# Performance work log

Hardware: AMD Instinct MI355X
Metric: run time of the kernel (lower is better)

## Reference

```python
import jax, jax.numpy as jnp
import numpy as np

D_MODEL = 512
NUM_HEADS = 8
D_K = D_MODEL // NUM_HEADS


def setup_inputs() -> dict:
    key = jax.random.key(0)
    ks = jax.random.split(key, 9)
    B, T = 4, 2048
    s = 1.0 / np.sqrt(D_MODEL)
    inp = {"x": jax.random.normal(ks[0], (B, T, D_MODEL), dtype=jnp.float32)}
    names = ["wq", "wk", "wv", "wo"]
    for i, n in enumerate(names):
        inp[n] = jax.random.uniform(ks[1 + i], (D_MODEL, D_MODEL), dtype=jnp.float32, minval=-s, maxval=s)
        inp["b" + n[1]] = jax.random.uniform(ks[5 + i], (D_MODEL,), dtype=jnp.float32, minval=-s, maxval=s)
    return inp


def reference(x, wq, bq, wk, bk, wv, bv, wo, bo):
    B, T, C = x.shape
    # Linear projections (torch Linear: x @ W^T + b)
    q = x @ wq.T + bq
    k = x @ wk.T + bk
    v = x @ wv.T + bv
    # [B, H, T, d_k]
    q = q.reshape(B, T, NUM_HEADS, D_K).transpose(0, 2, 1, 3)
    k = k.reshape(B, T, NUM_HEADS, D_K).transpose(0, 2, 1, 3)
    v = v.reshape(B, T, NUM_HEADS, D_K).transpose(0, 2, 1, 3)
    # scaled dot-product attention, full [B,H,T,T] scores materialized (faithful)
    scores = jnp.einsum('bhqd,bhkd->bhqk', q, k) / jnp.sqrt(jnp.float32(D_K))
    weights = jax.nn.softmax(scores, axis=-1)
    attn = jnp.einsum('bhqk,bhkd->bhqd', weights, v)
    attn = attn.transpose(0, 2, 1, 3).reshape(B, T, C)
    return attn @ wo.T + bo
```

## Files before the change

### kernel.cpp

```cpp
#include <hip/hip_runtime.h>

typedef __bf16 bf16x8 __attribute__((ext_vector_type(8)));
typedef __bf16 bf16x4 __attribute__((ext_vector_type(4)));
typedef float f32x4 __attribute__((ext_vector_type(4)));
typedef float f32x16 __attribute__((ext_vector_type(16)));

#define MFMA_16x16x32(a, b, c) __builtin_amdgcn_mfma_f32_16x16x32_bf16((a), (b), (c), 0, 0, 0)
#define MFMA32(a, b, c) __builtin_amdgcn_mfma_f32_32x32x16_bf16((a), (b), (c), 0, 0, 0)

#define WAIT_LGKM0() do { \
    asm volatile("s_waitcnt lgkmcnt(0)" ::: "memory"); \
    __builtin_amdgcn_sched_barrier(0); } while (0)

typedef const __attribute__((address_space(1))) void GVp;
typedef __attribute__((address_space(3))) void LVp;
#define GLOAD16(gp, lp) \
    __builtin_amdgcn_global_load_lds((GVp*)(gp), (LVp*)(lp), 16, 0, 0)

__device__ __forceinline__ float fexp2(float x) {
    float r;
    asm("v_exp_f32 %0, %1" : "=v"(r) : "v"(x));
    return r;
}

__device__ __forceinline__ unsigned cvtpk(float lo, float hi) {
    unsigned r;
    asm("v_cvt_pk_bf16_f32 %0, %1, %2" : "=v"(r) : "v"(lo), "v"(hi));
    return r;
}
#define PSWAP(a, b) asm volatile("v_permlane32_swap_b32 %0, %1" : "+v"(a), "+v"(b))

union PB { unsigned u[4]; bf16x8 v; };

__device__ __forceinline__ int swz(int row, int colb) {
    return row * 128 + (colb ^ ((row & 7) << 4));
}

__global__ __launch_bounds__(256) void cvt_all(const float* __restrict__ x,
                                               const float* __restrict__ w0,
                                               const float* __restrict__ w1,
                                               const float* __restrict__ w2,
                                               const float* __restrict__ w3,
                                               __bf16* __restrict__ xo,
                                               __bf16* __restrict__ o0,
                                               __bf16* __restrict__ o1,
                                               __bf16* __restrict__ o2,
                                               __bf16* __restrict__ o3) {
    int i = blockIdx.x * 256 + threadIdx.x;
    const float* in;
    __bf16* out;
    int idx;
    if (i < 1048576) {
        in = x; out = xo; idx = i;
    } else {
        int j = i - 1048576;
        int s = j >> 16;
        idx = j & 65535;
        in = (s == 0) ? w0 : (s == 1) ? w1 : (s == 2) ? w2 : w3;
        out = (s == 0) ? o0 : (s == 1) ? o1 : (s == 2) ? o2 : o3;
    }
    float4 v = ((const float4*)in)[idx];
    bf16x4 o;
    o[0] = (__bf16)v.x; o[1] = (__bf16)v.y; o[2] = (__bf16)v.z; o[3] = (__bf16)v.w;
    ((bf16x4*)out)[idx] = o;
}

template <typename OT, bool VT, int BN>
__device__ __forceinline__ void gemm_body(const __bf16* __restrict__ A,
                                          const __bf16* __restrict__ Bw,
                                          const float* __restrict__ bias,
                                          OT* __restrict__ C,
                                          int K, int N, float scale) {
    const int m0 = blockIdx.x * 128;
    const int n0 = blockIdx.y * BN;
    const int tid = threadIdx.x;
    const int l = tid & 63, w = tid >> 6;
    constexpr int MI = (BN == 128) ? 4 : 2;
    constexpr int WMS = (BN == 128) ? 64 : 32;
    const int wr = (BN == 128) ? (w >> 1) : w;
    const int wc = (BN == 128) ? (w & 1) : 0;
    const int lr = l & 15;
    const int lkb = (l >> 4) << 4;

    __shared__ __bf16 As[128 * 64];
    __shared__ __bf16 Bs[BN * 64];
    char* AsC = (char*)As;
    char* BsC = (char*)Bs;

    const int srow = tid >> 3;
    const int c8 = ((tid & 7) ^ (srow & 7)) * 8;

    f32x4 acc[MI][4] = {};

    for (int k0 = 0; k0 < K; k0 += 64) {
        __syncthreads();
#pragma unroll
        for (int p = 0; p < 4; ++p) {
            int row = p * 32 + srow;
            GLOAD16(A + (size_t)(m0 + row) * K + k0 + c8, AsC + p * 4096 + tid * 16);
        }
#pragma unroll
        for (int p = 0; p < BN / 32; ++p) {
            int row = p * 32 + srow;
            GLOAD16(Bw + (size_t)(n0 + row) * K + k0 + c8, BsC + p * 4096 + tid * 16);
        }
        __syncthreads();
#pragma unroll
        for (int kk = 0; kk < 2; ++kk) {
            bf16x8 af[MI], bfr[4];
#pragma unroll
            for (int mi = 0; mi < MI; ++mi)
                af[mi] = *(const bf16x8*)(AsC + swz(wr * WMS + mi * 16 + lr, kk * 64 + lkb));
#pragma unroll
            for (int ni = 0; ni < 4; ++ni)
                bfr[ni] = *(const bf16x8*)(BsC + swz(wc * 64 + ni * 16 + lr, kk * 64 + lkb));
#pragma unroll
            for (int mi = 0; mi < MI; ++mi)
#pragma unroll
                for (int ni = 0; ni < 4; ++ni)
                    acc[mi][ni] = MFMA_16x16x32(af[mi], bfr[ni], acc[mi][ni]);
        }
    }

    const int rb = (l >> 4) * 4;
#pragma unroll
    for (int mi = 0; mi < MI; ++mi) {
#pragma unroll
        for (int ni = 0; ni < 4; ++ni) {
            int gn = n0 + wc * 64 + ni * 16 + lr;
            int gm = m0 + wr * WMS + mi * 16 + rb;
            float bv = bias[gn];
            if constexpr (VT) {
                bf16x4 o4;
#pragma unroll
                for (int j = 0; j < 4; ++j)
                    o4[j] = (__bf16)((acc[mi][ni][j] + bv) * scale);
                *(bf16x4*)((__bf16*)C + ((size_t)(gm >> 11) << 20) +
                           (size_t)gn * 2048 + (gm & 2047)) = o4;
            } else {
#pragma unroll
                for (int j = 0; j < 4; ++j) {
                    float v = (acc[mi][ni][j] + bv) * scale;
                    C[(size_t)(gm + j) * N + gn] = (OT)v;
                }
            }
        }
    }
}

#define QSCALE 0.18033688f

__global__ __launch_bounds__(256) void qkv_gemm(const __bf16* __restrict__ X,
                                                const __bf16* __restrict__ Wq,
                                                const __bf16* __restrict__ Wk,
                                                const __bf16* __restrict__ Wv,
                                                const float* __restrict__ bq,
                                                const float* __restrict__ bk,
                                                const float* __restrict__ bv,
                                                __bf16* __restrict__ Qo,
                                                __bf16* __restrict__ Ko,
                                                __bf16* __restrict__ Vto) {
    int z = blockIdx.z;
    if (z == 0) {
        gemm_body<__bf16, false, 128>(X, Wq, bq, Qo, 512, 512, QSCALE);
    } else if (z == 1) {
        gemm_body<__bf16, false, 128>(X, Wk, bk, Ko, 512, 512, 1.0f);
    } else {
        gemm_body<__bf16, true, 128>(X, Wv, bv, Vto, 512, 512, 1.0f);
    }
}

__global__ __launch_bounds__(256) void out_gemm_fused(const __bf16* __restrict__ Op0,
                                                      const __bf16* __restrict__ Op1,
                                                      const float* __restrict__ lsum,
                                                      const __bf16* __restrict__ W,
                                                      const float* __restrict__ bias,
                                                      float* __restrict__ C) {
    const int m0 = blockIdx.x * 64;
    const int n0 = blockIdx.y * 128;
    const int tid = threadIdx.x;
    const int l = tid & 63, w = tid >> 6;
    const int wr = w >> 1, wc = w & 1;
    const int lr = l & 15;
    const int lkb = (l >> 4) << 4;

    __shared__ __bf16 As[64 * 64];
    __shared__ __bf16 Bs[128 * 64];
    __shared__ float2 wts[8][64];
    char* AsC = (char*)As;
    char* BsC = (char*)Bs;

    const int b = m0 >> 11, q0 = m0 & 2047;

#pragma unroll
    for (int j = 0; j < 2; ++j) {
        int idx = tid + j * 256;
        int i = idx & 63, hh = idx >> 6;
        size_t r = (size_t)(b * 8 + hh) * 2048 + q0 + i;
        float l0v = lsum[r], l1v = lsum[65536 + r];
        float inv = 1.f / (l0v + l1v);
        wts[hh][i] = make_float2(l0v * inv, l1v * inv);
    }

    const int srow = tid >> 3;
    const int c8 = ((tid & 7) ^ (srow & 7)) * 8;

    f32x4 acc[2][4] = {};

    for (int k0 = 0; k0 < 512; k0 += 64) {
        __syncthreads();
        const int hh = k0 >> 6;
#pragma unroll
        for (int p = 0; p < 2; ++p) {
            int row = p * 32 + srow;
            size_t r = (size_t)(b * 8 + hh) * 2048 + q0 + row;
            float2 wt = wts[hh][row];
            bf16x8 o0 = *(const bf16x8*)(Op0 + r * 64 + c8);
            bf16x8 o1 = *(const bf16x8*)(Op1 + r * 64 + c8);
            bf16x8 mg;
#pragma unroll
            for (int jj = 0; jj < 8; ++jj)
                mg[jj] = (__bf16)((float)o0[jj] * wt.x + (float)o1[jj] * wt.y);
            *(bf16x8*)(AsC + p * 4096 + tid * 16) = mg;
        }
#pragma unroll
        for (int p = 0; p < 4; ++p)
            GLOAD16(W + (size_t)(n0 + p * 32 + srow) * 512 + k0 + c8,
                    BsC + p * 4096 + tid * 16);
        __syncthreads();
#pragma unroll
        for (int kk = 0; kk < 2; ++kk) {
            bf16x8 af[2], bfr[4];
#pragma unroll
            for (int mi = 0; mi < 2; ++mi)
                af[mi] = *(const bf16x8*)(AsC + swz(wr * 32 + mi * 16 + lr, kk * 64 + lkb));
#pragma unroll
            for (int ni = 0; ni < 4; ++ni)
                bfr[ni] = *(const bf16x8*)(BsC + swz(wc * 64 + ni * 16 + lr, kk * 64 + lkb));
#pragma unroll
            for (int mi = 0; mi < 2; ++mi)
#pragma unroll
                for (int ni = 0; ni < 4; ++ni)
                    acc[mi][ni] = MFMA_16x16x32(af[mi], bfr[ni], acc[mi][ni]);
        }
    }

    const int rb = (l >> 4) * 4;
#pragma unroll
    for (int mi = 0; mi < 2; ++mi) {
#pragma unroll
        for (int ni = 0; ni < 4; ++ni) {
            int gn = n0 + wc * 64 + ni * 16 + lr;
            int gm = m0 + wr * 32 + mi * 16 + rb;
            float bv = bias[gn];
#pragma unroll
            for (int j = 0; j < 4; ++j)
                C[(size_t)(gm + j) * 512 + gn] = acc[mi][ni][j] + bv;
        }
    }
}

__global__ __launch_bounds__(256, 2) void attn_fwd(const __bf16* __restrict__ Q,
                                                   const __bf16* __restrict__ K,
                                                   const __bf16* __restrict__ Vt,
                                                   __bf16* __restrict__ Op0,
                                                   __bf16* __restrict__ Op1,
                                                   float* __restrict__ lsum) {
    const int T = 2048, Cm = 512;
    const int qt0 = blockIdx.x * 128;
    const int h = blockIdx.y;
    const int half = blockIdx.z & 1, b = blockIdx.z >> 1;
    const int kt0 = half * 1024, kend = kt0 + 1024;
    const int tid = threadIdx.x;
    const int l = tid & 63, w = tid >> 6;
    const int q5 = l & 31, hi = l >> 5;
    const size_t rbase = ((size_t)b * T) * Cm + h * 64;
    const size_t vtbase = ((size_t)b << 20) + (size_t)(h * 64) * 2048;

    __shared__ __align__(16) char smem[33280];

    const int grow = tid >> 3;
    const int gcol = ((tid & 7) ^ (grow & 7)) * 8;
    const __bf16* kgp = K + rbase + (size_t)grow * Cm + gcol;
    const __bf16* vgp = Vt + vtbase + (size_t)grow * 2048 + gcol;

#define ATTN_STAGE(nb, ktv)                                                   \
    do {                                                                      \
        char* kd_ = smem + (nb) * 8192 + tid * 16;                            \
        char* vd_ = smem + 16384 + (nb) * 8192 + tid * 16;                    \
        _Pragma("unroll")                                                     \
        for (int p = 0; p < 2; ++p) {                                         \
            GLOAD16(kgp + (size_t)((ktv) + p * 32) * Cm, kd_ + p * 4096);     \
            GLOAD16(vgp + (size_t)(p * 32) * 2048 + (ktv), vd_ + p * 4096);   \
        }                                                                     \
    } while (0)

    bf16x8 qf[4];
#pragma unroll
    for (int dc = 0; dc < 4; ++dc)
        qf[dc] = *(const bf16x8*)(Q + rbase +
            (size_t)(qt0 + w * 32 + q5) * Cm + dc * 16 + hi * 8);

    f32x16 oa[2] = {};
    float l_r = 0.f;

    ATTN_STAGE(0, kt0);
    __syncthreads();

    char* albase = smem + 32768 + w * 128;

    int cur = 0;
    for (int kt = kt0; kt < kend; kt += 64, cur ^= 1) {
        if (kt + 64 < kend) ATTN_STAGE(cur ^ 1, kt + 64);

        const char* kb_ = smem + cur * 8192;
        f32x16 s0 = {}, s1 = {};
#pragma unroll
        for (int dc = 0; dc < 4; ++dc) {
            bf16x8 kf0 = *(const bf16x8*)(kb_ + swz(q5, dc * 32 + hi * 16));
            bf16x8 kf1 = *(const bf16x8*)(kb_ + swz(32 + q5, dc * 32 + hi * 16));
            __builtin_amdgcn_s_setprio(1);
            s0 = MFMA32(kf0, qf[dc], s0);
            s1 = MFMA32(kf1, qf[dc], s1);
            __builtin_amdgcn_s_setprio(0);
        }

        float rs = 0.f;
#pragma unroll
        for (int r = 0; r < 16; ++r) {
            float p0 = fexp2(s0[r]);
            float p1 = fexp2(s1[r]);
            s0[r] = p0; s1[r] = p1;
            rs += p0 + p1;
        }
        rs += __shfl_xor(rs, 32);
        l_r += rs;

        PB pf[4];
#pragma unroll
        for (int kb = 0; kb < 2; ++kb) {
#pragma unroll
            for (int cc = 0; cc < 2; ++cc) {
                int gA = 8 * cc, gB = 8 * cc + 4;
                float a0, a1, a2, a3, b0, b1, b2, b3;
                if (kb == 0) {
                    a0 = s0[gA]; a1 = s0[gA + 1]; a2 = s0[gA + 2]; a3 = s0[gA + 3];
                    b0 = s0[gB]; b1 = s0[gB + 1]; b2 = s0[gB + 2]; b3 = s0[gB + 3];
                } else {
                    a0 = s1[gA]; a1 = s1[gA + 1]; a2 = s1[gA + 2]; a3 = s1[gA + 3];
                    b0 = s1[gB]; b1 = s1[gB + 1]; b2 = s1[gB + 2]; b3 = s1[gB + 3];
                }
                unsigned w0A = cvtpk(a0, a1), w1A = cvtpk(a2, a3);
                unsigned w0B = cvtpk(b0, b1), w1B = cvtpk(b2, b3);
                PSWAP(w0A, w0B);
                PSWAP(w1A, w1B);
                int kc = 2 * kb + cc;
                pf[kc].u[0] = w0A; pf[kc].u[1] = w1A;
                pf[kc].u[2] = w0B; pf[kc].u[3] = w1B;
            }
        }

        const char* vb_ = smem + 16384 + cur * 8192;
#pragma unroll
        for (int kc = 0; kc < 4; ++kc) {
            bf16x8 vf0 = *(const bf16x8*)(vb_ + swz(q5, kc * 32 + hi * 16));
            bf16x8 vf1 = *(const bf16x8*)(vb_ + swz(32 + q5, kc * 32 + hi * 16));
            __builtin_amdgcn_s_setprio(1);
            oa[0] = MFMA32(pf[kc].v, vf0, oa[0]);
            oa[1] = MFMA32(pf[kc].v, vf1, oa[1]);
            __builtin_amdgcn_s_setprio(0);
        }

        __syncthreads();
    }

    {
        float invl = 1.f / l_r;
        *(float*)(albase + q5 * 4) = invl;
        WAIT_LGKM0();
        f32x4 ivr[4];
#pragma unroll
        for (int rg = 0; rg < 4; ++rg)
            ivr[rg] = *(const f32x4*)(albase + hi * 16 + rg * 32);
        __bf16* Opb = half ? Op1 : Op0;
        const size_t rr = (size_t)(b * 8 + h) * 2048;
#pragma unroll
        for (int rg = 0; rg < 4; ++rg)
#pragma unroll
            for (int c = 0; c < 4; ++c) {
                int qr = qt0 + w * 32 + 8 * rg + 4 * hi + c;
                float iv = ivr[rg][c];
                Opb[(rr + qr) * 64 + q5]      = (__bf16)(oa[0][4 * rg + c] * iv);
                Opb[(rr + qr) * 64 + 32 + q5] = (__bf16)(oa[1][4 * rg + c] * iv);
            }
        if (hi == 0)
            lsum[(size_t)half * 65536 + rr + qt0 + w * 32 + q5] = l_r;
    }
#undef ATTN_STAGE
}

extern "C" void kernel_launch(void* const* d_in, const int* in_sizes, int n_in,
                              void* d_out, int out_size, void* d_ws, size_t ws_size,
                              hipStream_t stream) {
    const float* x  = (const float*)d_in[0];
    const float* wq = (const float*)d_in[1];
    const float* bq = (const float*)d_in[2];
    const float* wk = (const float*)d_in[3];
    const float* bk = (const float*)d_in[4];
    const float* wv = (const float*)d_in[5];
    const float* bv = (const float*)d_in[6];
    const float* wo = (const float*)d_in[7];
    const float* bo = (const float*)d_in[8];

    char* ws = (char*)d_ws;
    __bf16* xb    = (__bf16*)(ws);
    __bf16* Op0   = (__bf16*)(ws);
    __bf16* Qb    = (__bf16*)(ws + ((size_t)8 << 20));
    __bf16* Kb    = (__bf16*)(ws + ((size_t)16 << 20));
    __bf16* Vtb   = (__bf16*)(ws + ((size_t)24 << 20));
    __bf16* Op1   = (__bf16*)(ws + ((size_t)32 << 20));
    __bf16* wqb   = (__bf16*)(ws + ((size_t)40 << 20));
    __bf16* wkb   = (__bf16*)(ws + ((size_t)40 << 20) + ((size_t)512 << 10));
    __bf16* wvb   = (__bf16*)(ws + ((size_t)40 << 20) + ((size_t)1024 << 10));
    __bf16* wob   = (__bf16*)(ws + ((size_t)40 << 20) + ((size_t)1536 << 10));
    float*  lsb   = (float*)(ws + ((size_t)42 << 20));

    cvt_all<<<dim3(5120), dim3(256), 0, stream>>>(x, wq, wk, wv, wo,
                                                  xb, wqb, wkb, wvb, wob);
    qkv_gemm<<<dim3(64, 4, 3), dim3(256), 0, stream>>>(xb, wqb, wkb, wvb,
                                                       bq, bk, bv, Qb, Kb, Vtb);
    attn_fwd<<<dim3(16, 8, 8), dim3(256), 0, stream>>>(Qb, Kb, Vtb, Op0, Op1, lsb);
    out_gemm_fused<<<dim3(128, 4), dim3(256), 0, stream>>>(Op0, Op1, lsb, wob, bo,
                                                           (float*)d_out);
}
```

Measured before the change: 94.13 us.

## Load K/V attention fragments directly from global memory, drop LDS staging

```diff
diff --git a/kernel.cpp b/kernel.cpp
--- a/kernel.cpp
+++ b/kernel.cpp
@@ -260,7 +260,7 @@
     }
 }
 
-__global__ __launch_bounds__(256, 2) void attn_fwd(const __bf16* __restrict__ Q,
+__global__ __launch_bounds__(256, 4) void attn_fwd(const __bf16* __restrict__ Q,
                                                    const __bf16* __restrict__ K,
                                                    const __bf16* __restrict__ Vt,
                                                    __bf16* __restrict__ Op0,
@@ -270,30 +270,14 @@
     const int qt0 = blockIdx.x * 128;
     const int h = blockIdx.y;
     const int half = blockIdx.z & 1, b = blockIdx.z >> 1;
-    const int kt0 = half * 1024, kend = kt0 + 1024;
+    const int kt0 = half * 1024;
     const int tid = threadIdx.x;
     const int l = tid & 63, w = tid >> 6;
     const int q5 = l & 31, hi = l >> 5;
     const size_t rbase = ((size_t)b * T) * Cm + h * 64;
     const size_t vtbase = ((size_t)b << 20) + (size_t)(h * 64) * 2048;
 
-    __shared__ __align__(16) char smem[33280];
-
-    const int grow = tid >> 3;
-    const int gcol = ((tid & 7) ^ (grow & 7)) * 8;
-    const __bf16* kgp = K + rbase + (size_t)grow * Cm + gcol;
-    const __bf16* vgp = Vt + vtbase + (size_t)grow * 2048 + gcol;
-
-#define ATTN_STAGE(nb, ktv)                                                   \
-    do {                                                                      \
-        char* kd_ = smem + (nb) * 8192 + tid * 16;                            \
-        char* vd_ = smem + 16384 + (nb) * 8192 + tid * 16;                    \
-        _Pragma("unroll")                                                     \
-        for (int p = 0; p < 2; ++p) {                                         \
-            GLOAD16(kgp + (size_t)((ktv) + p * 32) * Cm, kd_ + p * 4096);     \
-            GLOAD16(vgp + (size_t)(p * 32) * 2048 + (ktv), vd_ + p * 4096);   \
-        }                                                                     \
-    } while (0)
+    __shared__ __align__(16) char smem[512];
 
     bf16x8 qf[4];
 #pragma unroll
@@ -301,27 +285,28 @@
         qf[dc] = *(const bf16x8*)(Q + rbase +
             (size_t)(qt0 + w * 32 + q5) * Cm + dc * 16 + hi * 8);
 
+    const __bf16* kq0 = K + rbase + (size_t)(kt0 + q5) * Cm + hi * 8;
+    const __bf16* kq1 = kq0 + (size_t)32 * Cm;
+    const __bf16* vq0 = Vt + vtbase + (size_t)q5 * 2048 + kt0 + hi * 8;
+    const __bf16* vq1 = vq0 + (size_t)32 * 2048;
+
     f32x16 oa[2] = {};
     float l_r = 0.f;
-
-    ATTN_STAGE(0, kt0);
-    __syncthreads();
-
-    char* albase = smem + 32768 + w * 128;
-
-    int cur = 0;
-    for (int kt = kt0; kt < kend; kt += 64, cur ^= 1) {
-        if (kt + 64 < kend) ATTN_STAGE(cur ^ 1, kt + 64);
-
-        const char* kb_ = smem + cur * 8192;
+    char* albase = smem + w * 128;
+
+    for (int it = 0; it < 16; ++it) {
+        bf16x8 kf0[4], kf1[4];
+#pragma unroll
+        for (int dc = 0; dc < 4; ++dc) {
+            kf0[dc] = *(const bf16x8*)(kq0 + dc * 16);
+            kf1[dc] = *(const bf16x8*)(kq1 + dc * 16);
+        }
         f32x16 s0 = {}, s1 = {};
 #pragma unroll
         for (int dc = 0; dc < 4; ++dc) {
-            bf16x8 kf0 = *(const bf16x8*)(kb_ + swz(q5, dc * 32 + hi * 16));
-            bf16x8 kf1 = *(const bf16x8*)(kb_ + swz(32 + q5, dc * 32 + hi * 16));
             __builtin_amdgcn_s_setprio(1);
-            s0 = MFMA32(kf0, qf[dc], s0);
-            s1 = MFMA32(kf1, qf[dc], s1);
+            s0 = MFMA32(kf0[dc], qf[dc], s0);
+            s1 = MFMA32(kf1[dc], qf[dc], s1);
             __builtin_amdgcn_s_setprio(0);
         }
 
@@ -360,18 +345,24 @@
             }
         }
 
-        const char* vb_ = smem + 16384 + cur * 8192;
+        bf16x8 vf0[4], vf1[4];
 #pragma unroll
         for (int kc = 0; kc < 4; ++kc) {
-            bf16x8 vf0 = *(const bf16x8*)(vb_ + swz(q5, kc * 32 + hi * 16));
-            bf16x8 vf1 = *(const bf16x8*)(vb_ + swz(32 + q5, kc * 32 + hi * 16));
+            vf0[kc] = *(const bf16x8*)(vq0 + kc * 16);
+            vf1[kc] = *(const bf16x8*)(vq1 + kc * 16);
+        }
+#pragma unroll
+        for (int kc = 0; kc < 4; ++kc) {
             __builtin_amdgcn_s_setprio(1);
-            oa[0] = MFMA32(pf[kc].v, vf0, oa[0]);
-            oa[1] = MFMA32(pf[kc].v, vf1, oa[1]);
+            oa[0] = MFMA32(pf[kc].v, vf0[kc], oa[0]);
+            oa[1] = MFMA32(pf[kc].v, vf1[kc], oa[1]);
             __builtin_amdgcn_s_setprio(0);
         }
 
-        __syncthreads();
+        kq0 += (size_t)64 * Cm;
+        kq1 += (size_t)64 * Cm;
+        vq0 += 64;
+        vq1 += 64;
     }
 
     {
@@ -396,7 +387,6 @@
         if (hi == 0)
             lsum[(size_t)half * 65536 + rr + qt0 + w * 32 + q5] = l_r;
     }
-#undef ATTN_STAGE
 }
 
 extern "C" void kernel_launch(void* const* d_in, const int* in_sizes, int n_in,
```

Result: slower. 165.0 us (+75.3%).
